# Performance work log

Hardware: AMD Instinct MI355X
Metric: run time of the kernel (lower is better)

## Reference

```python
import jax, jax.numpy as jnp
import numpy as np

B, L, D, H = 2, 2048, 1024, 16
HD = D // H  # head size = 64


def setup_inputs() -> dict:
    key = jax.random.key(0)
    ks = jax.random.split(key, 7)
    scale = 0.02
    return {
        "queries": jax.random.normal(ks[0], (B, L, D), dtype=jnp.float32),
        "keys": jax.random.normal(ks[1], (B, L, D), dtype=jnp.float32),
        "values": jax.random.normal(ks[2], (B, L, D), dtype=jnp.float32),
        "Wq": jax.random.normal(ks[3], (D, D), dtype=jnp.float32) * scale,
        "Wk": jax.random.normal(ks[4], (D, D), dtype=jnp.float32) * scale,
        "Wv": jax.random.normal(ks[5], (D, D), dtype=jnp.float32) * scale,
        "Wo": jax.random.normal(ks[6], (D, D), dtype=jnp.float32) * scale,
    }


def _split_heads(x):
    # (B, L, D) -> (B, H, L, HD); matches torch's transpose/view head split
    b, l, d = x.shape
    return x.reshape(b, l, H, HD).transpose(0, 2, 1, 3)


def reference(queries, keys, values, Wq, Wk, Wv, Wo):
    q = _split_heads(queries @ Wq.T)  # (B,H,Lq,HD)
    k = _split_heads(keys @ Wk.T)     # (B,H,Lk,HD)
    v = _split_heads(values @ Wv.T)   # (B,H,Lk,HD)

    scaling = jax.lax.rsqrt(jnp.float32(HD))
    scores = scaling * jnp.einsum("bhqd,bhkd->bhqk", q, k)  # (B,H,Lq,Lk)

    # Faithful to source quirk: mask = tril(scores); scores[mask == 0] = -inf.
    # This masks the strict upper triangle AND any lower-tri score exactly 0.
    tril_scores = jnp.tril(scores)
    scores = jnp.where(tril_scores == 0, -jnp.inf, scores)

    attention = jax.nn.softmax(scores, axis=-1)  # (B,H,Lq,Lk)

    context = jnp.einsum("bhqk,bhkd->bhqd", attention, v)  # (B,H,Lq,HD)
    context = context.transpose(0, 2, 1, 3).reshape(B, L, D)
    context = context @ Wo.T  # (B,Lq,D)
    return attention, context
```

## Files before the change

kernel.cpp:

```cpp
#include <hip/hip_runtime.h>
#include <hip/hip_bf16.h>

#define LL 2048
#define DD 1024
#define HH 16

typedef __attribute__((ext_vector_type(8))) short short8;
typedef __attribute__((ext_vector_type(4))) float floatx4;

#define OFF_XQ 0ul
#define OFF_XK 4194304ul
#define OFF_XV 8388608ul
#define OFF_WQ 12582912ul
#define OFF_WK 13631488ul
#define OFF_WV 14680064ul
#define OFF_WO 15728640ul
#define OFF_QH 16777216ul
#define OFF_KH 20971520ul
#define OFF_VT 25165824ul
#define OFF_CT 29360128ul

__device__ __forceinline__ unsigned short f2bf(float f) {
  union { float f; unsigned int u; } v; v.f = f;
  unsigned int r = v.u + 0x7fffu + ((v.u >> 16) & 1u);
  return (unsigned short)(r >> 16);
}

__device__ __forceinline__ short8 pack8(float4 a, float4 b) {
  short8 s;
  s[0]=(short)f2bf(a.x); s[1]=(short)f2bf(a.y); s[2]=(short)f2bf(a.z); s[3]=(short)f2bf(a.w);
  s[4]=(short)f2bf(b.x); s[5]=(short)f2bf(b.y); s[6]=(short)f2bf(b.z); s[7]=(short)f2bf(b.w);
  return s;
}

#define GLOAD_LDS16(g, l)                                            \
  __builtin_amdgcn_global_load_lds(                                  \
      (const __attribute__((address_space(1))) void*)(g),            \
      (__attribute__((address_space(3))) void*)(l), 16, 0, 0)

__global__ __launch_bounds__(256) void k_cvt(
    const float* __restrict__ x0, const float* __restrict__ x1, const float* __restrict__ x2,
    const float* __restrict__ w0, const float* __restrict__ w1, const float* __restrict__ w2,
    const float* __restrict__ w3, unsigned short* __restrict__ ws)
{
  const int y = blockIdx.y;
  const float* src; unsigned short* dst; int n;
  switch (y) {
    case 0: src = x0; dst = ws + OFF_XQ; n = 4194304; break;
    case 1: src = x1; dst = ws + OFF_XK; n = 4194304; break;
    case 2: src = x2; dst = ws + OFF_XV; n = 4194304; break;
    case 3: src = w0; dst = ws + OFF_WQ; n = 1048576; break;
    case 4: src = w1; dst = ws + OFF_WK; n = 1048576; break;
    case 5: src = w2; dst = ws + OFF_WV; n = 1048576; break;
    default: src = w3; dst = ws + OFF_WO; n = 1048576; break;
  }
  int i = (blockIdx.x * 256 + threadIdx.x) * 8;
  if (i >= n) return;
  const float4* p = reinterpret_cast<const float4*>(src + i);
  *reinterpret_cast<short8*>(dst + i) = pack8(p[0], p[1]);
}

template<int MODE>
__global__ __launch_bounds__(256) void k_gemm(
    const unsigned short* __restrict__ A,
    const unsigned short* __restrict__ B,
    void* __restrict__ dstv)
{
  const int I0 = blockIdx.x * 128;
  const int N0 = blockIdx.y * 64;
  const int tid = threadIdx.x;
  const int lane = tid & 63;
  const int w = tid >> 6;
  const int wr = w >> 1, wc = w & 1;
  const int colb = lane & 15;
  const int rowb = (lane >> 4) * 4;
  const int kseg = (lane >> 4) * 8;

  __shared__ unsigned short Abuf[128 * 64];
  __shared__ unsigned short Bbuf[64 * 64];

  floatx4 acc[4][2] = {};

  for (int k0 = 0; k0 < DD; k0 += 64) {
#pragma unroll
    for (int i = 0; i < 4; ++i) {
      int e = (i * 4 + w) * 512 + lane * 8;
      const unsigned short* g = A + (size_t)(I0 + (e >> 6)) * DD + k0 + (e & 63);
      GLOAD_LDS16(g, Abuf + (i * 4 + w) * 512);
    }
#pragma unroll
    for (int i = 0; i < 2; ++i) {
      int e = (i * 4 + w) * 512 + lane * 8;
      const unsigned short* g = B + (size_t)(N0 + (e >> 6)) * DD + k0 + (e & 63);
      GLOAD_LDS16(g, Bbuf + (i * 4 + w) * 512);
    }
    __syncthreads();
#pragma unroll
    for (int kk = 0; kk < 2; ++kk) {
      short8 ar[4], br[2];
#pragma unroll
      for (int mi = 0; mi < 4; ++mi)
        ar[mi] = *reinterpret_cast<const short8*>(
            &Abuf[(wr * 64 + mi * 16 + colb) * 64 + kk * 32 + kseg]);
#pragma unroll
      for (int ni = 0; ni < 2; ++ni)
        br[ni] = *reinterpret_cast<const short8*>(
            &Bbuf[(wc * 32 + ni * 16 + colb) * 64 + kk * 32 + kseg]);
#pragma unroll
      for (int mi = 0; mi < 4; ++mi)
#pragma unroll
        for (int ni = 0; ni < 2; ++ni)
          acc[mi][ni] = __builtin_amdgcn_mfma_f32_16x16x32_bf16(ar[mi], br[ni], acc[mi][ni], 0, 0, 0);
    }
    __syncthreads();
  }

#pragma unroll
  for (int mi = 0; mi < 4; ++mi) {
#pragma unroll
    for (int ni = 0; ni < 2; ++ni) {
      int col = N0 + wc * 32 + ni * 16 + colb;
#pragma unroll
      for (int rr = 0; rr < 4; ++rr) {
        int row = I0 + wr * 64 + mi * 16 + rowb + rr;
        if (MODE == 3) {
          ((float*)dstv)[(size_t)row * DD + col] = acc[mi][ni][rr];
        } else {
          unsigned short val = f2bf(acc[mi][ni][rr]);
          int h = col >> 6, hd = col & 63;
          int b = row >> 11, l = row & 2047;
          unsigned short* dst = (unsigned short*)dstv;
          if (MODE == 0)
            dst[(((size_t)(b * HH + h)) * LL + l) * 64 + hd] = val;
          else
            dst[(((size_t)(b * HH + h)) * 64 + hd) * LL + l] = val;
        }
      }
    }
  }
}

__global__ __launch_bounds__(256) void k_attn(
    const unsigned short* __restrict__ Qh,
    const unsigned short* __restrict__ Kh,
    const unsigned short* __restrict__ Vt,
    float* __restrict__ attn,
    unsigned short* __restrict__ Ctx)
{
  const int qt = blockIdx.x;
  const int bh = blockIdx.y;
  const int b = bh >> 4, h = bh & 15;
  const int Q0 = qt * 64;
  const int tid = threadIdx.x;
  const int lane = tid & 63;
  const int w = tid >> 6;
  const int colb = lane & 15;
  const int rowb = (lane >> 4) * 4;
  const int kseg = (lane >> 4) * 8;
  const float scale = 0.125f;

  __shared__ float Pf[4][16 * 68];
  unsigned short* Plw = (unsigned short*)&Pf[w][0];
  float* Pfw = &Pf[w][0];

  const unsigned short* Qbase = Qh + (size_t)bh * LL * 64;
  const unsigned short* Kbase = Kh + (size_t)bh * LL * 64;
  const unsigned short* Vbase = Vt + (size_t)bh * 64 * LL;

  const int qrow = Q0 + w * 16 + colb;
  short8 qf0 = *reinterpret_cast<const short8*>(Qbase + (size_t)qrow * 64 + kseg);
  short8 qf1 = *reinterpret_cast<const short8*>(Qbase + (size_t)qrow * 64 + 32 + kseg);

  short8 ones;
#pragma unroll
  for (int j = 0; j < 8; ++j) ones[j] = (short)0x3F80;

  floatx4 ssum = {};
  floatx4 cacc[4] = {};

  for (int kt = 0; kt <= qt; ++kt) {
    const int K0 = kt * 64;
    floatx4 sacc[4] = {};
#pragma unroll
    for (int nt = 0; nt < 4; ++nt) {
      const unsigned short* kp = Kbase + (size_t)(K0 + nt * 16 + colb) * 64 + kseg;
      short8 kf0 = *reinterpret_cast<const short8*>(kp);
      short8 kf1 = *reinterpret_cast<const short8*>(kp + 32);
      sacc[nt] = __builtin_amdgcn_mfma_f32_16x16x32_bf16(qf0, kf0, sacc[nt], 0, 0, 0);
      sacc[nt] = __builtin_amdgcn_mfma_f32_16x16x32_bf16(qf1, kf1, sacc[nt], 0, 0, 0);
    }
#pragma unroll
    for (int nt = 0; nt < 4; ++nt) {
      int col = K0 + nt * 16 + colb;
#pragma unroll
      for (int rr = 0; rr < 4; ++rr) {
        int row = Q0 + w * 16 + rowb + rr;
        float sv = sacc[nt][rr] * scale;
        float e = ((col > row) || (sv == 0.0f)) ? 0.0f : __expf(sv);
        Plw[(rowb + rr) * 72 + nt * 16 + colb] = f2bf(e);
      }
    }
#pragma unroll
    for (int s = 0; s < 2; ++s) {
      short8 pf = *reinterpret_cast<const short8*>(&Plw[colb * 72 + s * 32 + kseg]);
      ssum = __builtin_amdgcn_mfma_f32_16x16x32_bf16(pf, ones, ssum, 0, 0, 0);
#pragma unroll
      for (int nt = 0; nt < 4; ++nt) {
        const unsigned short* vp = Vbase + (size_t)(nt * 16 + colb) * LL + K0 + s * 32 + kseg;
        short8 vf = *reinterpret_cast<const short8*>(vp);
        cacc[nt] = __builtin_amdgcn_mfma_f32_16x16x32_bf16(pf, vf, cacc[nt], 0, 0, 0);
      }
    }
  }

  float inv[4];
#pragma unroll
  for (int rr = 0; rr < 4; ++rr) inv[rr] = 1.0f / ssum[rr];

#pragma unroll
  for (int nt = 0; nt < 4; ++nt) {
    int col = h * 64 + nt * 16 + colb;
#pragma unroll
    for (int rr = 0; rr < 4; ++rr) {
      int row = Q0 + w * 16 + rowb + rr;
      Ctx[((size_t)b * LL + row) * DD + col] = f2bf(cacc[nt][rr] * inv[rr]);
    }
  }

  for (int kt = 0; kt <= qt; ++kt) {
    const int K0 = kt * 64;
    floatx4 sacc[4] = {};
#pragma unroll
    for (int nt = 0; nt < 4; ++nt) {
      const unsigned short* kp = Kbase + (size_t)(K0 + nt * 16 + colb) * 64 + kseg;
      short8 kf0 = *reinterpret_cast<const short8*>(kp);
      short8 kf1 = *reinterpret_cast<const short8*>(kp + 32);
      sacc[nt] = __builtin_amdgcn_mfma_f32_16x16x32_bf16(qf0, kf0, sacc[nt], 0, 0, 0);
      sacc[nt] = __builtin_amdgcn_mfma_f32_16x16x32_bf16(qf1, kf1, sacc[nt], 0, 0, 0);
    }
#pragma unroll
    for (int nt = 0; nt < 4; ++nt) {
      int col = K0 + nt * 16 + colb;
#pragma unroll
      for (int rr = 0; rr < 4; ++rr) {
        int row = Q0 + w * 16 + rowb + rr;
        float sv = sacc[nt][rr] * scale;
        float p = ((col > row) || (sv == 0.0f)) ? 0.0f : __expf(sv) * inv[rr];
        Pfw[(rowb + rr) * 68 + nt * 16 + colb] = p;
      }
    }
#pragma unroll
    for (int i = 0; i < 4; ++i) {
      int idx = i * 64 + lane;
      int prow = idx >> 4, c4 = idx & 15;
      float4 v = *reinterpret_cast<const float4*>(&Pfw[prow * 68 + c4 * 4]);
      *reinterpret_cast<float4*>(
          &attn[((size_t)bh * LL + Q0 + w * 16 + prow) * LL + K0 + c4 * 4]) = v;
    }
  }

  const int C0 = (qt + 1) * 64;
  if (C0 < LL) {
    const int zl4 = (LL - C0) >> 2;
    const float4 z = make_float4(0.f, 0.f, 0.f, 0.f);
    for (int row = 0; row < 64; ++row) {
      float4* dst = reinterpret_cast<float4*>(attn + ((size_t)bh * LL + Q0 + row) * LL + C0);
      for (int c = tid; c < zl4; c += 256) dst[c] = z;
    }
  }
}

extern "C" void kernel_launch(void* const* d_in, const int* in_sizes, int n_in,
                              void* d_out, int out_size, void* d_ws, size_t ws_size,
                              hipStream_t stream) {
  const float* q  = (const float*)d_in[0];
  const float* k  = (const float*)d_in[1];
  const float* v  = (const float*)d_in[2];
  const float* wq = (const float*)d_in[3];
  const float* wk = (const float*)d_in[4];
  const float* wv = (const float*)d_in[5];
  const float* wo = (const float*)d_in[6];

  float* attn   = (float*)d_out;
  float* ctxout = (float*)d_out + (size_t)32 * LL * LL;

  unsigned short* ws = (unsigned short*)d_ws;

  k_cvt<<<dim3(2048, 7), 256, 0, stream>>>(q, k, v, wq, wk, wv, wo, ws);
  k_gemm<0><<<dim3(32, 16), 256, 0, stream>>>(ws + OFF_XQ, ws + OFF_WQ, ws + OFF_QH);
  k_gemm<0><<<dim3(32, 16), 256, 0, stream>>>(ws + OFF_XK, ws + OFF_WK, ws + OFF_KH);
  k_gemm<2><<<dim3(32, 16), 256, 0, stream>>>(ws + OFF_XV, ws + OFF_WV, ws + OFF_VT);
  k_attn<<<dim3(32, 32), 256, 0, stream>>>(ws + OFF_QH, ws + OFF_KH, ws + OFF_VT, attn, ws + OFF_CT);
  k_gemm<3><<<dim3(32, 16), 256, 0, stream>>>(ws + OFF_CT, ws + OFF_WO, ctxout);
}
```

Before: 970.3 us.

## Fuse QKV projections into one launch with 128x128 swizzled-LDS GEMM tiles

Merges the three projection GEMMs into a single launch indexed by panel and enlarges the output tile from 128x64 to 128x128, with an XOR swizzle on LDS chunk placement to avoid bank conflicts. The output projection uses the same tiling. In attention, the scale and natural-exp pair is replaced by exp2f with a folded log2e*scale constant. The aim is less launch overhead, more reuse per loaded tile and cheaper LDS reads, at the cost of more accumulator registers per thread and fewer blocks in the output GEMM.

```diff
diff --git a/kernel.cpp b/kernel.cpp
--- a/kernel.cpp
+++ b/kernel.cpp
@@ -60,81 +60,159 @@
   *reinterpret_cast<short8*>(dst + i) = pack8(p[0], p[1]);
 }
 
-template<int MODE>
-__global__ __launch_bounds__(256) void k_gemm(
-    const unsigned short* __restrict__ A,
-    const unsigned short* __restrict__ B,
-    void* __restrict__ dstv)
+__global__ __launch_bounds__(256) void k_qkv(unsigned short* __restrict__ ws)
 {
+  const int panel = blockIdx.y >> 3;
+  const int N0 = (blockIdx.y & 7) * 128;
   const int I0 = blockIdx.x * 128;
-  const int N0 = blockIdx.y * 64;
+
+  const unsigned short* A = ws + (panel == 0 ? OFF_XQ : panel == 1 ? OFF_XK : OFF_XV);
+  const unsigned short* B = ws + (panel == 0 ? OFF_WQ : panel == 1 ? OFF_WK : OFF_WV);
+
   const int tid = threadIdx.x;
   const int lane = tid & 63;
   const int w = tid >> 6;
   const int wr = w >> 1, wc = w & 1;
   const int colb = lane & 15;
-  const int rowb = (lane >> 4) * 4;
-  const int kseg = (lane >> 4) * 8;
+  const int grp = lane >> 4;
+  const int rowb = grp * 4;
 
   __shared__ unsigned short Abuf[128 * 64];
-  __shared__ unsigned short Bbuf[64 * 64];
-
-  floatx4 acc[4][2] = {};
+  __shared__ unsigned short Bbuf[128 * 64];
+
+  floatx4 acc[4][4] = {};
+  const int sr = tid >> 3;
+  const int sch = tid & 7;
 
   for (int k0 = 0; k0 < DD; k0 += 64) {
 #pragma unroll
     for (int i = 0; i < 4; ++i) {
-      int e = (i * 4 + w) * 512 + lane * 8;
-      const unsigned short* g = A + (size_t)(I0 + (e >> 6)) * DD + k0 + (e & 63);
-      GLOAD_LDS16(g, Abuf + (i * 4 + w) * 512);
-    }
-#pragma unroll
-    for (int i = 0; i < 2; ++i) {
-      int e = (i * 4 + w) * 512 + lane * 8;
-      const unsigned short* g = B + (size_t)(N0 + (e >> 6)) * DD + k0 + (e & 63);
-      GLOAD_LDS16(g, Bbuf + (i * 4 + w) * 512);
+      int r = i * 32 + sr;
+      GLOAD_LDS16(A + (size_t)(I0 + r) * DD + k0 + ((sch ^ (r & 7)) * 8),
+                  Abuf + i * 2048 + w * 512);
+    }
+#pragma unroll
+    for (int i = 0; i < 4; ++i) {
+      int r = i * 32 + sr;
+      GLOAD_LDS16(B + (size_t)(N0 + r) * DD + k0 + ((sch ^ (r & 7)) * 8),
+                  Bbuf + i * 2048 + w * 512);
     }
     __syncthreads();
 #pragma unroll
     for (int kk = 0; kk < 2; ++kk) {
-      short8 ar[4], br[2];
+      short8 af[4], bf[4];
+#pragma unroll
+      for (int mi = 0; mi < 4; ++mi) {
+        int row = wr * 64 + mi * 16 + colb;
+        af[mi] = *reinterpret_cast<const short8*>(
+            &Abuf[row * 64 + ((kk * 4 + grp) ^ (row & 7)) * 8]);
+      }
+#pragma unroll
+      for (int ni = 0; ni < 4; ++ni) {
+        int row = wc * 64 + ni * 16 + colb;
+        bf[ni] = *reinterpret_cast<const short8*>(
+            &Bbuf[row * 64 + ((kk * 4 + grp) ^ (row & 7)) * 8]);
+      }
 #pragma unroll
       for (int mi = 0; mi < 4; ++mi)
-        ar[mi] = *reinterpret_cast<const short8*>(
-            &Abuf[(wr * 64 + mi * 16 + colb) * 64 + kk * 32 + kseg]);
-#pragma unroll
-      for (int ni = 0; ni < 2; ++ni)
-        br[ni] = *reinterpret_cast<const short8*>(
-            &Bbuf[(wc * 32 + ni * 16 + colb) * 64 + kk * 32 + kseg]);
-#pragma unroll
-      for (int mi = 0; mi < 4; ++mi)
-#pragma unroll
-        for (int ni = 0; ni < 2; ++ni)
-          acc[mi][ni] = __builtin_amdgcn_mfma_f32_16x16x32_bf16(ar[mi], br[ni], acc[mi][ni], 0, 0, 0);
+#pragma unroll
+        for (int ni = 0; ni < 4; ++ni)
+          acc[mi][ni] = __builtin_amdgcn_mfma_f32_16x16x32_bf16(af[mi], bf[ni], acc[mi][ni], 0, 0, 0);
     }
     __syncthreads();
   }
 
+  unsigned short* dstQK = ws + (panel == 0 ? OFF_QH : OFF_KH);
+  unsigned short* dstV = ws + OFF_VT;
 #pragma unroll
   for (int mi = 0; mi < 4; ++mi) {
 #pragma unroll
-    for (int ni = 0; ni < 2; ++ni) {
-      int col = N0 + wc * 32 + ni * 16 + colb;
+    for (int ni = 0; ni < 4; ++ni) {
+      int c = N0 + wc * 64 + ni * 16 + colb;
+      int h = c >> 6, hd = c & 63;
 #pragma unroll
       for (int rr = 0; rr < 4; ++rr) {
         int row = I0 + wr * 64 + mi * 16 + rowb + rr;
-        if (MODE == 3) {
-          ((float*)dstv)[(size_t)row * DD + col] = acc[mi][ni][rr];
-        } else {
-          unsigned short val = f2bf(acc[mi][ni][rr]);
-          int h = col >> 6, hd = col & 63;
-          int b = row >> 11, l = row & 2047;
-          unsigned short* dst = (unsigned short*)dstv;
-          if (MODE == 0)
-            dst[(((size_t)(b * HH + h)) * LL + l) * 64 + hd] = val;
-          else
-            dst[(((size_t)(b * HH + h)) * 64 + hd) * LL + l] = val;
-        }
+        int b = row >> 11, l = row & 2047;
+        unsigned short val = f2bf(acc[mi][ni][rr]);
+        if (panel < 2)
+          dstQK[(((size_t)(b * HH + h)) * LL + l) * 64 + hd] = val;
+        else
+          dstV[(((size_t)(b * HH + h)) * 64 + hd) * LL + l] = val;
+      }
+    }
+  }
+}
+
+__global__ __launch_bounds__(256) void k_out(
+    const unsigned short* __restrict__ Ctx, const unsigned short* __restrict__ Wo,
+    float* __restrict__ Out)
+{
+  const int N0 = blockIdx.y * 128;
+  const int I0 = blockIdx.x * 128;
+
+  const int tid = threadIdx.x;
+  const int lane = tid & 63;
+  const int w = tid >> 6;
+  const int wr = w >> 1, wc = w & 1;
+  const int colb = lane & 15;
+  const int grp = lane >> 4;
+  const int rowb = grp * 4;
+
+  __shared__ unsigned short Abuf[128 * 64];
+  __shared__ unsigned short Bbuf[128 * 64];
+
+  floatx4 acc[4][4] = {};
+  const int sr = tid >> 3;
+  const int sch = tid & 7;
+
+  for (int k0 = 0; k0 < DD; k0 += 64) {
+#pragma unroll
+    for (int i = 0; i < 4; ++i) {
+      int r = i * 32 + sr;
+      GLOAD_LDS16(Ctx + (size_t)(I0 + r) * DD + k0 + ((sch ^ (r & 7)) * 8),
+                  Abuf + i * 2048 + w * 512);
+    }
+#pragma unroll
+    for (int i = 0; i < 4; ++i) {
+      int r = i * 32 + sr;
+      GLOAD_LDS16(Wo + (size_t)(N0 + r) * DD + k0 + ((sch ^ (r & 7)) * 8),
+                  Bbuf + i * 2048 + w * 512);
+    }
+    __syncthreads();
+#pragma unroll
+    for (int kk = 0; kk < 2; ++kk) {
+      short8 af[4], bf[4];
+#pragma unroll
+      for (int mi = 0; mi < 4; ++mi) {
+        int row = wr * 64 + mi * 16 + colb;
+        af[mi] = *reinterpret_cast<const short8*>(
+            &Abuf[row * 64 + ((kk * 4 + grp) ^ (row & 7)) * 8]);
+      }
+#pragma unroll
+      for (int ni = 0; ni < 4; ++ni) {
+        int row = wc * 64 + ni * 16 + colb;
+        bf[ni] = *reinterpret_cast<const short8*>(
+            &Bbuf[row * 64 + ((kk * 4 + grp) ^ (row & 7)) * 8]);
+      }
+#pragma unroll
+      for (int mi = 0; mi < 4; ++mi)
+#pragma unroll
+        for (int ni = 0; ni < 4; ++ni)
+          acc[mi][ni] = __builtin_amdgcn_mfma_f32_16x16x32_bf16(af[mi], bf[ni], acc[mi][ni], 0, 0, 0);
+    }
+    __syncthreads();
+  }
+
+#pragma unroll
+  for (int mi = 0; mi < 4; ++mi) {
+#pragma unroll
+    for (int ni = 0; ni < 4; ++ni) {
+      int col = N0 + wc * 64 + ni * 16 + colb;
+#pragma unroll
+      for (int rr = 0; rr < 4; ++rr) {
+        int row = I0 + wr * 64 + mi * 16 + rowb + rr;
+        Out[(size_t)row * DD + col] = acc[mi][ni][rr];
       }
     }
   }
@@ -157,7 +235,7 @@
   const int colb = lane & 15;
   const int rowb = (lane >> 4) * 4;
   const int kseg = (lane >> 4) * 8;
-  const float scale = 0.125f;
+  const float CE = 0.18033688011112042f;
 
   __shared__ float Pf[4][16 * 68];
   unsigned short* Plw = (unsigned short*)&Pf[w][0];
@@ -195,8 +273,8 @@
 #pragma unroll
       for (int rr = 0; rr < 4; ++rr) {
         int row = Q0 + w * 16 + rowb + rr;
-        float sv = sacc[nt][rr] * scale;
-        float e = ((col > row) || (sv == 0.0f)) ? 0.0f : __expf(sv);
+        float raw = sacc[nt][rr];
+        float e = ((col > row) || (raw == 0.0f)) ? 0.0f : exp2f(raw * CE);
         Plw[(rowb + rr) * 72 + nt * 16 + colb] = f2bf(e);
       }
     }
@@ -244,8 +322,8 @@
 #pragma unroll
       for (int rr = 0; rr < 4; ++rr) {
         int row = Q0 + w * 16 + rowb + rr;
-        float sv = sacc[nt][rr] * scale;
-        float p = ((col > row) || (sv == 0.0f)) ? 0.0f : __expf(sv) * inv[rr];
+        float raw = sacc[nt][rr];
+        float p = ((col > row) || (raw == 0.0f)) ? 0.0f : exp2f(raw * CE) * inv[rr];
         Pfw[(rowb + rr) * 68 + nt * 16 + colb] = p;
       }
     }
@@ -287,9 +365,7 @@
   unsigned short* ws = (unsigned short*)d_ws;
 
   k_cvt<<<dim3(2048, 7), 256, 0, stream>>>(q, k, v, wq, wk, wv, wo, ws);
-  k_gemm<0><<<dim3(32, 16), 256, 0, stream>>>(ws + OFF_XQ, ws + OFF_WQ, ws + OFF_QH);
-  k_gemm<0><<<dim3(32, 16), 256, 0, stream>>>(ws + OFF_XK, ws + OFF_WK, ws + OFF_KH);
-  k_gemm<2><<<dim3(32, 16), 256, 0, stream>>>(ws + OFF_XV, ws + OFF_WV, ws + OFF_VT);
+  k_qkv<<<dim3(32, 24), 256, 0, stream>>>(ws);
   k_attn<<<dim3(32, 32), 256, 0, stream>>>(ws + OFF_QH, ws + OFF_KH, ws + OFF_VT, attn, ws + OFF_CT);
-  k_gemm<3><<<dim3(32, 16), 256, 0, stream>>>(ws + OFF_CT, ws + OFF_WO, ctxout);
-}
+  k_out<<<dim3(32, 8), 256, 0, stream>>>(ws + OFF_CT, ws + OFF_WO, ctxout);
+}
```

Result: faster. 946.9 us (-2.4%).
